# Kernel tuning notes

Hardware: AMD Instinct MI355X
Metric: run time of the kernel (lower is better)

## Reference

```python
import jax, jax.numpy as jnp
import numpy as np

BS, NQ, NC = 128, 900, 91
PRE_TOPK = 10000      # source: pre_topk when n_queries*n_cls > 10000
POST_TOPK = 100       # source: keep_inds[:100]
IOU_THRESH = 0.7


def box_cxcywh_to_xyxy(b):
    cx, cy, w, h = b[..., 0], b[..., 1], b[..., 2], b[..., 3]
    return jnp.stack([cx - 0.5 * w, cy - 0.5 * h, cx + 0.5 * w, cy + 0.5 * h], axis=-1)


def nms_image(boxes, scores, labels):
    """Greedy batched NMS, returning the first POST_TOPK picked indices.
    boxes: [PRE,4] xyxy (scaled), scores: [PRE] desc-sorted, labels: [PRE] int.
    batched_nms trick: offset boxes per class so IoU across classes is 0."""
    max_coord = jnp.max(boxes)
    off = labels.astype(boxes.dtype) * (max_coord + 1.0)
    ob = boxes + off[:, None]                          # [PRE,4]
    areas = (ob[:, 2] - ob[:, 0]) * (ob[:, 3] - ob[:, 1])

    def step(active, _):
        s = jnp.where(active, scores, -jnp.inf)
        i = jnp.argmax(s)                              # highest-score surviving box
        bi = ob[i]
        xx1 = jnp.maximum(bi[0], ob[:, 0])
        yy1 = jnp.maximum(bi[1], ob[:, 1])
        xx2 = jnp.minimum(bi[2], ob[:, 2])
        yy2 = jnp.minimum(bi[3], ob[:, 3])
        inter = jnp.clip(xx2 - xx1, 0.0) * jnp.clip(yy2 - yy1, 0.0)
        union = areas[i] + areas - inter
        iou = inter / jnp.maximum(union, 1e-9)
        # suppress IoU > thresh (includes i itself since iou(i,i)=1)
        active = active & (iou <= IOU_THRESH)
        return active, i

    _, keep = jax.lax.scan(step, jnp.ones(ob.shape[0], dtype=bool), None, length=POST_TOPK)
    return keep                                         # [POST]


def setup_inputs() -> dict:
    key = jax.random.key(0)
    k1, k2, k3, k4 = jax.random.split(key, 4)
    pred_logits = jax.random.normal(k1, (BS, NQ, NC), dtype=jnp.float32) * 2.0 - 2.0
    cxcy = jax.random.uniform(k2, (BS, NQ, 2), dtype=jnp.float32)
    wh = jax.random.uniform(k3, (BS, NQ, 2), dtype=jnp.float32, minval=0.02, maxval=0.3)
    pred_boxes = jnp.concatenate([cxcy, wh], axis=-1)   # cxcywh in [0,1]
    target_sizes = jax.random.uniform(k4, (BS, 2), dtype=jnp.float32, minval=480.0, maxval=1333.0)
    return {"pred_logits": pred_logits, "pred_boxes": pred_boxes, "target_sizes": target_sizes}


def reference(pred_logits, pred_boxes, target_sizes):
    bs, nq, nc = pred_logits.shape
    prob = jax.nn.sigmoid(pred_logits).reshape(bs, nq * nc)      # all_scores
    boxes = box_cxcywh_to_xyxy(pred_boxes)                        # [bs,nq,4]
    img_h, img_w = target_sizes[:, 0], target_sizes[:, 1]
    scale = jnp.stack([img_w, img_h, img_w, img_h], axis=1)       # [bs,4]
    boxes = boxes * scale[:, None, :]

    top_scores, top_idx = jax.lax.top_k(prob, PRE_TOPK)           # [bs,PRE]
    top_labels = top_idx % nc                                     # all_labels gather
    top_box_idx = top_idx // nc                                   # all_boxes gather
    top_boxes = jnp.take_along_axis(boxes, top_box_idx[..., None], axis=1)  # [bs,PRE,4]

    keep = jax.vmap(nms_image)(top_boxes, top_scores, top_labels)  # [bs,POST]
    out_scores = jnp.take_along_axis(top_scores, keep, axis=1)
    out_labels = jnp.take_along_axis(top_labels, keep, axis=1)
    out_boxes = jnp.take_along_axis(top_boxes, keep[..., None], axis=1)
    return out_scores, out_labels, out_boxes
```

## Files before the change

kernel.cpp:

```cpp
#include <hip/hip_runtime.h>
#include <cstdint>

#pragma clang fp contract(off)

#define BS   128
#define NQ   900
#define NC   91
#define NQC  (NQ * NC)
#define Q4   (NQC / 4)
#define HHALF 10238
#define PRE  10000
#define POST 100
#define TBITS 13
#define TBINS (1 << TBITS)
#define TSHIFT (32 - TBITS)
#define K_WIN 16
#define HSEG 1024
#define KS   2780
#define CAPH 7680
#define NSLOT 15

typedef unsigned long long ull;

#define WS_CNT 0
#define WS_GH  4096
#define WS_KEYS (4096 + 4*1024*1024)

__device__ __forceinline__ uint32_t fkey(float f) {
    uint32_t b = __float_as_uint(f);
    return (b & 0x80000000u) ? ~b : (b | 0x80000000u);
}
__device__ __forceinline__ float unkey(uint32_t u) {
    uint32_t b = (u & 0x80000000u) ? (u & 0x7FFFFFFFu) : ~u;
    return __uint_as_float(b);
}
__device__ __forceinline__ uint32_t qclamp(uint32_t q) { return (q < NQ) ? q : (NQ - 1); }

__device__ __forceinline__ ull shflx(ull v, int j) {
    uint32_t lo = (uint32_t)__shfl_xor((int)(uint32_t)v, j, 64);
    uint32_t hi = (uint32_t)__shfl_xor((int)(uint32_t)(v >> 32), j, 64);
    return ((ull)hi << 32) | (ull)lo;
}
__device__ __forceinline__ ull cex(ull v, int j, bool lower, bool desc) {
    ull pb = shflx(v, j);
    ull a = lower ? v : pb;
    ull b = lower ? pb : v;
    bool sw = desc ? (a < b) : (a > b);
    return sw ? pb : v;
}
__device__ __forceinline__ void ce(ull& a, ull& b, bool desc) {
    bool sw = desc ? (a < b) : (a > b);
    if (sw) { ull t = a; a = b; b = t; }
}

__global__ void __launch_bounds__(1024) k_compact(const float* __restrict__ logits,
                                                  ull* __restrict__ keys,
                                                  uint16_t* __restrict__ ghist,
                                                  uint32_t* __restrict__ cnts) {
    const int img = blockIdx.x >> 1;
    const int h = blockIdx.x & 1;
    const int tid = threadIdx.x;
    const int lane = tid & 63;
    __shared__ uint32_t hist[TBINS];
    __shared__ uint32_t part[1024];
    __shared__ uint32_t sTB, sCnt;
    const float4* lg4 = (const float4*)(logits + (size_t)img * NQC);
    for (int i = tid; i < TBINS; i += 1024) hist[i] = 0u;
    if (tid == 0) sCnt = 0u;
    float4 sv[5];
    #pragma unroll
    for (int c = 0; c < 5; ++c) sv[c] = lg4[c * 4096 + tid];
    __syncthreads();
    #pragma unroll
    for (int c = 0; c < 5; ++c) {
        atomicAdd(&hist[fkey(sv[c].x) >> TSHIFT], 1u);
        atomicAdd(&hist[fkey(sv[c].y) >> TSHIFT], 1u);
        atomicAdd(&hist[fkey(sv[c].z) >> TSHIFT], 1u);
        atomicAdd(&hist[fkey(sv[c].w) >> TSHIFT], 1u);
    }
    __syncthreads();
    {
        uint32_t s = 0;
        int b0 = tid * 8;
        #pragma unroll
        for (int j = 0; j < 8; ++j) s += hist[b0 + j];
        part[tid] = s;
    }
    __syncthreads();
    if (tid < 64) {
        uint32_t pv[16]; uint32_t tot = 0;
        #pragma unroll
        for (int j = 0; j < 16; ++j) { pv[j] = part[tid * 16 + j]; tot += pv[j]; }
        uint32_t sinc = tot;
        #pragma unroll
        for (int off = 1; off < 64; off <<= 1) {
            uint32_t o = (uint32_t)__shfl_down((int)sinc, off, 64);
            if (tid + off < 64) sinc += o;
        }
        uint32_t cum = sinc - tot;
        for (int j = 15; j >= 0; --j) {
            if (cum < KS && cum + pv[j] >= KS) {
                int pbn = (tid * 16 + j) * 8;
                uint32_t c2 = cum;
                for (int b = pbn + 7; b >= pbn; --b) {
                    if (c2 + hist[b] >= KS) { sTB = (uint32_t)b; break; }
                    c2 += hist[b];
                }
            }
            cum += pv[j];
        }
    }
    __syncthreads();
    const uint32_t TB = sTB;
    for (int i = tid; i < TBINS; i += 1024) hist[i] = 0u;
    __syncthreads();
    ull* seg = keys + (size_t)(img * 2 + h) * CAPH;
    const int lo = h * HHALF;
    const int hi = (lo + HHALF < Q4) ? (lo + HHALF) : Q4;
    for (int i0 = lo; i0 < hi; i0 += 4096) {
        float4 v[4]; bool inb[4]; int ii[4];
        #pragma unroll
        for (int s = 0; s < 4; ++s) {
            int i = i0 + (s << 10) + tid;
            ii[s] = i; inb[s] = (i < hi);
            v[s] = inb[s] ? lg4[i] : make_float4(0.f, 0.f, 0.f, 0.f);
        }
        uint32_t u[16]; bool pass[16];
        #pragma unroll
        for (int s = 0; s < 4; ++s) {
            u[s * 4 + 0] = fkey(v[s].x); u[s * 4 + 1] = fkey(v[s].y);
            u[s * 4 + 2] = fkey(v[s].z); u[s * 4 + 3] = fkey(v[s].w);
            #pragma unroll
            for (int c = 0; c < 4; ++c)
                pass[s * 4 + c] = inb[s] && ((u[s * 4 + c] >> TSHIFT) >= TB);
        }
        ull m[16]; uint32_t pc[16]; uint32_t tot = 0;
        #pragma unroll
        for (int c = 0; c < 16; ++c) {
            m[c] = __ballot(pass[c]);
            pc[c] = (uint32_t)__popcll(m[c]);
            tot += pc[c];
        }
        uint32_t wb = 0u;
        if (lane == 0 && tot) wb = atomicAdd(&sCnt, tot);
        wb = (uint32_t)__shfl((int)wb, 0, 64);
        ull lm = (1ull << lane) - 1ull;
        uint32_t off = 0;
        #pragma unroll
        for (int c = 0; c < 16; ++c) {
            if (pass[c]) {
                uint32_t p = wb + off + (uint32_t)__popcll(m[c] & lm);
                uint32_t fi = (uint32_t)(ii[c >> 2] * 4 + (c & 3));
                if (p < CAPH) {
                    seg[p] = ((ull)u[c] << 32) | (ull)(0xFFFFFFFFu - fi);
                    atomicAdd(&hist[u[c] >> TSHIFT], 1u);
                }
            }
            off += pc[c];
        }
    }
    __syncthreads();
    uint16_t* g = ghist + (size_t)(img * 2 + h) * TBINS;
    for (int i = tid; i < TBINS; i += 1024) g[i] = (uint16_t)hist[i];
    if (tid == 0) cnts[img * 2 + h] = (sCnt < CAPH) ? sCnt : CAPH;
}

__global__ void __launch_bounds__(1024) k_sel(const ull* __restrict__ keys,
                                              const uint16_t* __restrict__ ghist,
                                              const uint32_t* __restrict__ cnts,
                                              const float* __restrict__ pred_boxes,
                                              const float* __restrict__ target_sizes,
                                              float* __restrict__ out) {
    const int img = blockIdx.x;
    const int tid = threadIdx.x;
    const int lane = tid & 63;
    const int wv = tid >> 6;

    __shared__ uint32_t hist[TBINS];
    __shared__ uint32_t part[1024];
    __shared__ float4 shPB[NQ];
    __shared__ ull binK[HSEG];
    __shared__ ull headK[HSEG];
    __shared__ float aX1[POST], aY1[POST], aX2[POST], aY2[POST], aAr[POST];
    __shared__ int   aCl[POST];
    __shared__ float s_x1[K_WIN], s_y1[K_WIN], s_x2[K_WIN], s_y2[K_WIN];
    __shared__ int   s_cl[K_WIN];
    __shared__ uint32_t s_em[K_WIN];
    __shared__ ull sF0;
    __shared__ uint32_t sCntA, sCntB, sMX;
    __shared__ uint32_t sB1, sTp1, sB2, sTp2, sTK;

    const float ih = target_sizes[img * 2 + 0];
    const float iw = target_sizes[img * 2 + 1];
    const float* pb = pred_boxes + (size_t)img * NQ * 4;

    auto mckey = [&](uint32_t f) -> uint32_t {
        uint32_t q = qclamp(f / NC);
        float4 bb = shPB[q];
        float x1 = (bb.x - 0.5f * bb.z) * iw;
        float y1 = (bb.y - 0.5f * bb.w) * ih;
        float x2 = (bb.x + 0.5f * bb.z) * iw;
        float y2 = (bb.y + 0.5f * bb.w) * ih;
        return fkey(fmaxf(fmaxf(x1, y1), fmaxf(x2, y2)));
    };

    if (tid < NQ) shPB[tid] = ((const float4*)pb)[tid];
    binK[tid] = 0ull; headK[tid] = 0ull;
    if (tid == 0) { sCntA = 0u; sCntB = 0u; sMX = 0u; sF0 = 0ull;
                    sB1 = 0u; sTp1 = 1u; sB2 = 0u; sTp2 = 0u; sTK = 0u; }
    {
        const uint16_t* g0 = ghist + (size_t)(img * 2) * TBINS;
        const uint16_t* g1 = g0 + TBINS;
        uint32_t s = 0;
        int b0 = tid * 8;
        #pragma unroll
        for (int j = 0; j < 8; ++j) {
            uint32_t hv = (uint32_t)g0[b0 + j] + (uint32_t)g1[b0 + j];
            hist[b0 + j] = hv;
            s += hv;
        }
        part[tid] = s;
    }
    const uint32_t c0 = cnts[img * 2 + 0];
    const uint32_t c1 = cnts[img * 2 + 1];
    const int total = (int)(c0 + c1);
    const ull* seg0 = keys + (size_t)(img * 2) * CAPH;
    const ull* seg1 = seg0 + CAPH;
    ull kk[NSLOT];
    #pragma unroll
    for (int j = 0; j < NSLOT; ++j) {
        int i = tid + (j << 10);
        ull x = 0ull;
        if (i < total) x = (i < (int)c0) ? seg0[i] : seg1[i - (int)c0];
        kk[j] = x;
    }
    __syncthreads();

    if (tid < 64) {
        uint32_t pv[16]; uint32_t tot = 0;
        #pragma unroll
        for (int j = 0; j < 16; ++j) { pv[j] = part[tid * 16 + j]; tot += pv[j]; }
        uint32_t sinc = tot;
        #pragma unroll
        for (int off = 1; off < 64; off <<= 1) {
            uint32_t o = (uint32_t)__shfl_down((int)sinc, off, 64);
            if (tid + off < 64) sinc += o;
        }
        uint32_t tt = (uint32_t)__shfl((int)sinc, 0, 64);
        uint32_t TKl = (tt < PRE) ? tt : PRE;
        uint32_t T2l = (TKl < HSEG) ? TKl : HSEG;
        if (tid == 0) sTK = TKl;
        uint32_t cum = sinc - tot;
        for (int j = 15; j >= 0; --j) {
            if (cum < TKl && cum + pv[j] >= TKl) {
                int pbn = (tid * 16 + j) * 8;
                uint32_t c2 = cum;
                for (int b = pbn + 7; b >= pbn; --b) {
                    if (c2 + hist[b] >= TKl) { sB1 = (uint32_t)b; sTp1 = TKl - c2; break; }
                    c2 += hist[b];
                }
            }
            if (cum < T2l && cum + pv[j] >= T2l) {
                int pbn = (tid * 16 + j) * 8;
                uint32_t c2 = cum;
                for (int b = pbn + 7; b >= pbn; --b) {
                    if (c2 + hist[b] >= T2l) { sB2 = (uint32_t)b; sTp2 = T2l - c2; break; }
                    c2 += hist[b];
                }
            }
            cum += pv[j];
        }
    }
    __syncthreads();
    const uint32_t B1 = sB1, tp1 = sTp1, B2 = sB2;
    const uint32_t TK = sTK;
    const int C1 = (int)(((TK < (uint32_t)HSEG) ? TK : (uint32_t)HSEG) - sTp2);

    uint32_t lmx = 0u;
    {
        uint32_t cA = 0u, cB = 0u;
        #pragma unroll
        for (int j = 0; j < NSLOT; ++j) {
            ull x = kk[j];
            uint32_t bin = (uint32_t)(x >> 51);
            bool liveK = (x != 0ull);
            if (liveK && bin > B1) { uint32_t km = mckey(~(uint32_t)x); if (km > lmx) lmx = km; }
            cA += (liveK && bin == B1) ? 1u : 0u;
            cB += (liveK && bin > B2) ? 1u : 0u;
        }
        uint32_t rA = cA, rB = cB;
        #pragma unroll
        for (int off = 32; off > 0; off >>= 1) {
            rA += (uint32_t)__shfl_down((int)rA, off, 64);
            rB += (uint32_t)__shfl_down((int)rB, off, 64);
        }
        if (lane == 0) { part[wv] = rA; part[16 + wv] = rB; }
        __syncthreads();
        if (tid == 0) {
            uint32_t sA = 0u, sB = 0u;
            #pragma unroll
            for (int w = 0; w < 16; ++w) {
                part[32 + w] = sA; sA += part[w];
                part[48 + w] = sB; sB += part[16 + w];
            }
        }
        __syncthreads();
        uint32_t curA = part[32 + wv];
        uint32_t curB = part[48 + wv];
        ull lm = (1ull << lane) - 1ull;
        #pragma unroll
        for (int j = 0; j < NSLOT; ++j) {
            ull x = kk[j];
            uint32_t bin = (uint32_t)(x >> 51);
            bool liveK = (x != 0ull);
            bool isA = liveK && (bin == B1);
            bool isB = liveK && (bin > B2);
            ull mA = __ballot(isA);
            ull mB = __ballot(isB);
            if (isA) {
                uint32_t p = curA + (uint32_t)__popcll(mA & lm);
                if (p < HSEG) binK[p] = x;
            }
            if (isB) {
                uint32_t p = curB + (uint32_t)__popcll(mB & lm);
                if (p < HSEG) headK[p] = x;
            }
            curA += (uint32_t)__popcll(mA);
            curB += (uint32_t)__popcll(mB);
        }
    }
    __syncthreads();

    {
        ull r0 = 0, r1 = 0, r2 = 0, r3 = 0;
        const int cw = wv & 3;
        const int cb = cw << 8;
        ull* A = (wv < 4) ? binK : headK;
        if (wv < 8) {
            r0 = A[cb | lane]; r1 = A[cb | 64 | lane];
            r2 = A[cb | 128 | lane]; r3 = A[cb | 192 | lane];
            #pragma unroll
            for (int k2 = 2; k2 <= 32; k2 <<= 1) {
                bool d = ((lane & k2) == 0);
                #pragma unroll
                for (int j = 16; j >= 1; j >>= 1) {
                    if (j <= (k2 >> 1)) {
                        bool lw = ((lane & j) == 0);
                        r0 = cex(r0, j, lw, d); r1 = cex(r1, j, lw, d);
                        r2 = cex(r2, j, lw, d); r3 = cex(r3, j, lw, d);
                    }
                }
            }
            #pragma unroll
            for (int j = 32; j >= 1; j >>= 1) {
                bool lw = ((lane & j) == 0);
                r0 = cex(r0, j, lw, true);  r1 = cex(r1, j, lw, false);
                r2 = cex(r2, j, lw, true);  r3 = cex(r3, j, lw, false);
            }
            ce(r0, r1, true); ce(r2, r3, false);
            #pragma unroll
            for (int j = 32; j >= 1; j >>= 1) {
                bool lw = ((lane & j) == 0);
                r0 = cex(r0, j, lw, true);  r1 = cex(r1, j, lw, true);
                r2 = cex(r2, j, lw, false); r3 = cex(r3, j, lw, false);
            }
            {
                bool d = ((cw & 1) == 0);
                ce(r0, r2, d); ce(r1, r3, d); ce(r0, r1, d); ce(r2, r3, d);
                #pragma unroll
                for (int j = 32; j >= 1; j >>= 1) {
                    bool lw = ((lane & j) == 0);
                    r0 = cex(r0, j, lw, d); r1 = cex(r1, j, lw, d);
                    r2 = cex(r2, j, lw, d); r3 = cex(r3, j, lw, d);
                }
            }
            A[cb | lane] = r0; A[cb | 64 | lane] = r1;
            A[cb | 128 | lane] = r2; A[cb | 192 | lane] = r3;
        }
        __syncthreads();
        {
            ull* Bp = (tid >> 9) ? headK : binK;
            int t = tid & 511;
            int i = ((t & ~255) << 1) | (t & 255);
            int ixj = i | 256;
            bool d = ((i & 512) == 0);
            ull a = Bp[i], b = Bp[ixj];
            bool sw = d ? (a < b) : (a > b);
            if (sw) { Bp[i] = b; Bp[ixj] = a; }
        }
        __syncthreads();
        if (wv < 8) {
            r0 = A[cb | lane]; r1 = A[cb | 64 | lane];
            r2 = A[cb | 128 | lane]; r3 = A[cb | 192 | lane];
            bool d = ((cw & 2) == 0);
            ce(r0, r2, d); ce(r1, r3, d); ce(r0, r1, d); ce(r2, r3, d);
            #pragma unroll
            for (int j = 32; j >= 1; j >>= 1) {
                bool lw = ((lane & j) == 0);
                r0 = cex(r0, j, lw, d); r1 = cex(r1, j, lw, d);
                r2 = cex(r2, j, lw, d); r3 = cex(r3, j, lw, d);
            }
            A[cb | lane] = r0; A[cb | 64 | lane] = r1;
            A[cb | 128 | lane] = r2; A[cb | 192 | lane] = r3;
        }
        __syncthreads();
        {
            ull* Bp = (tid >> 9) ? headK : binK;
            int t = tid & 511;
            ull a = Bp[t], b = Bp[t | 512];
            if (a < b) { Bp[t] = b; Bp[t | 512] = a; }
        }
        __syncthreads();
        {
            ull* Bp = (tid >> 9) ? headK : binK;
            int t = tid & 511;
            int i = ((t & ~255) << 1) | (t & 255);
            int ixj = i | 256;
            ull a = Bp[i], b = Bp[ixj];
            if (a < b) { Bp[i] = b; Bp[ixj] = a; }
        }
        __syncthreads();
        if (wv < 8) {
            r0 = A[cb | lane]; r1 = A[cb | 64 | lane];
            r2 = A[cb | 128 | lane]; r3 = A[cb | 192 | lane];
            ce(r0, r2, true); ce(r1, r3, true); ce(r0, r1, true); ce(r2, r3, true);
            #pragma unroll
            for (int j = 32; j >= 1; j >>= 1) {
                bool lw = ((lane & j) == 0);
                r0 = cex(r0, j, lw, true); r1 = cex(r1, j, lw, true);
                r2 = cex(r2, j, lw, true); r3 = cex(r3, j, lw, true);
            }
            A[cb | lane] = r0; A[cb | 64 | lane] = r1;
            A[cb | 128 | lane] = r2; A[cb | 192 | lane] = r3;
        }
        __syncthreads();
    }

    if (tid < (int)tp1) {
        ull x = binK[tid];
        if (x != 0ull) { uint32_t km = mckey(~(uint32_t)x); if (km > lmx) lmx = km; }
    }
    for (int off = 32; off > 0; off >>= 1) {
        uint32_t o = (uint32_t)__shfl_down((int)lmx, off, 64);
        if (o > lmx) lmx = o;
    }
    if (lane == 0) atomicMax(&sMX, lmx);
    if (tid == 0 && C1 > 0) sF0 = headK[0];
    __syncthreads();
    float offD;
    {
        uint32_t m = sMX;
        uint32_t b = (m & 0x80000000u) ? (m & 0x7FFFFFFFu) : ~m;
        offD = __uint_as_float(b) + 1.0f;
    }

    auto sort1024 = [&]() {
        const int idx = tid;
        ull x = headK[idx];
        #pragma unroll
        for (int k2 = 2; k2 <= 32; k2 <<= 1) {
            bool d = ((lane & k2) == 0);
            #pragma unroll
            for (int j = 16; j >= 1; j >>= 1)
                if (j <= (k2 >> 1)) x = cex(x, j, (lane & j) == 0, d);
        }
        {
            bool d = ((idx & 64) == 0);
            #pragma unroll
            for (int j = 32; j >= 1; j >>= 1) x = cex(x, j, (lane & j) == 0, d);
        }
        for (int k = 128; k <= 1024; k <<= 1) {
            headK[idx] = x;
            __syncthreads();
            for (int j = k >> 1; j >= 64; j >>= 1) {
                if (tid < 512) {
                    int i2 = ((tid & ~(j - 1)) << 1) | (tid & (j - 1));
                    int ixj = i2 | j;
                    ull a = headK[i2], b = headK[ixj];
                    bool sw = ((i2 & k) == 0) ? (a < b) : (a > b);
                    if (sw) { headK[i2] = b; headK[ixj] = a; }
                }
                __syncthreads();
            }
            x = headK[idx];
            bool d = ((idx & k) == 0);
            #pragma unroll
            for (int j = 32; j >= 1; j >>= 1) x = cex(x, j, (lane & j) == 0, d);
        }
        headK[idx] = x;
        __syncthreads();
    };

    int npick = 0, base = 0, segbase = 0, segend = C1;
    int bcur = (int)B2;
    bool needF0 = (C1 == 0);
    while (npick < POST) {
        if (base >= segend) {
            if (segend >= (int)TK) {
                ull x0 = sF0;
                uint32_t f0 = ~(uint32_t)x0;
                uint32_t u0 = (uint32_t)(x0 >> 32);
                uint32_t q0 = qclamp(f0 / NC);
                uint32_t cc0 = f0 - (f0 / NC) * NC;
                float4 bb = shPB[q0];
                float rx1 = (bb.x - 0.5f * bb.z) * iw;
                float ry1 = (bb.y - 0.5f * bb.w) * ih;
                float rx2 = (bb.x + 0.5f * bb.z) * iw;
                float ry2 = (bb.y + 0.5f * bb.w) * ih;
                float sc = 1.0f / (1.0f + expf(-unkey(u0)));
                for (int p2 = npick + tid; p2 < POST; p2 += 1024) {
                    out[img * POST + p2] = sc;
                    out[BS * POST + img * POST + p2] = (float)cc0;
                    float* ob2 = out + 2 * BS * POST + ((size_t)img * POST + p2) * 4;
                    ob2[0] = rx1; ob2[1] = ry1; ob2[2] = rx2; ob2[3] = ry2;
                }
                break;
            }
            while (bcur > 0 && hist[bcur] == 0u) --bcur;
            headK[tid] = 0ull;
            if (tid == 0) sCntA = 0u;
            __syncthreads();
            for (int i0 = 0; i0 < total; i0 += 1024) {
                int i = i0 + tid;
                ull x = 0ull;
                if (i < total) x = (i < (int)c0) ? seg0[i] : seg1[i - (int)c0];
                bool pass = (x != 0ull) && ((uint32_t)(x >> 51) == (uint32_t)bcur);
                ull m = __ballot(pass);
                if (m) {
                    uint32_t wb = 0u;
                    if (lane == 0) wb = atomicAdd(&sCntA, (uint32_t)__popcll(m));
                    wb = (uint32_t)__shfl((int)wb, 0, 64);
                    if (pass) {
                        uint32_t p = wb + (uint32_t)__popcll(m & ((1ull << lane) - 1ull));
                        if (p < HSEG) headK[p] = x;
                    }
                }
            }
            __syncthreads();
            sort1024();
            int avail = (int)((sCntA < (uint32_t)HSEG) ? sCntA : (uint32_t)HSEG);
            int take = (int)TK - segend; if (take > avail) take = avail;
            if (needF0) { if (tid == 0) sF0 = headK[0]; needF0 = false; __syncthreads(); }
            segbase = segend; segend += take; --bcur;
            continue;
        }

        const int r = base + wv;
        const bool val = (r < segend);
        const ull xk = headK[val ? (r - segbase) : 0];
        const uint32_t f = val ? ~(uint32_t)xk : 0u;
        const uint32_t uk = (uint32_t)(xk >> 32);
        const uint32_t q = qclamp(f / NC);
        const uint32_t cc = f - (f / NC) * NC;
        float4 bb = shPB[q];
        const float x1 = (bb.x - 0.5f * bb.z) * iw;
        const float y1 = (bb.y - 0.5f * bb.w) * ih;
        const float x2 = (bb.x + 0.5f * bb.z) * iw;
        const float y2 = (bb.y + 0.5f * bb.w) * ih;
        if (lane == 0) {
            s_x1[wv] = x1; s_y1[wv] = y1; s_x2[wv] = x2; s_y2[wv] = y2;
            s_cl[wv] = val ? (int)cc : -1;
        }
        __syncthreads();

        const float o = (float)cc * offD;
        const float cx1 = x1 + o, cy1 = y1 + o, cx2 = x2 + o, cy2 = y2 + o;
        const float car = (cx2 - cx1) * (cy2 - cy1);
        bool cf = false;
        if (val && lane < wv && s_cl[lane] == (int)cc) {
            float jx1 = s_x1[lane] + o, jy1 = s_y1[lane] + o;
            float jx2 = s_x2[lane] + o, jy2 = s_y2[lane] + o;
            float arj = (jx2 - jx1) * (jy2 - jy1);
            float xx1 = fmaxf(jx1, cx1), yy1 = fmaxf(jy1, cy1);
            float xx2 = fminf(jx2, cx2), yy2 = fminf(jy2, cy2);
            float inter = fmaxf(xx2 - xx1, 0.0f) * fmaxf(yy2 - yy1, 0.0f);
            float uni = (arj + car) - inter;
            float iou = inter / fmaxf(uni, 1e-9f);
            cf = !(iou <= 0.7f);
        }
        uint32_t em = (uint32_t)(__ballot(cf) & 0xFFFFull);
        bool pf = false;
        for (int i2 = lane; i2 < npick; i2 += 64) {
            if (aCl[i2] == (int)cc) {
                float jx1 = aX1[i2] + o, jy1 = aY1[i2] + o;
                float jx2 = aX2[i2] + o, jy2 = aY2[i2] + o;
                float arj = aAr[i2];
                float xx1 = fmaxf(jx1, cx1), yy1 = fmaxf(jy1, cy1);
                float xx2 = fminf(jx2, cx2), yy2 = fminf(jy2, cy2);
                float inter = fmaxf(xx2 - xx1, 0.0f) * fmaxf(yy2 - yy1, 0.0f);
                float uni = (arj + car) - inter;
                float iou = inter / fmaxf(uni, 1e-9f);
                pf |= !(iou <= 0.7f);
            }
        }
        bool anyPrior = (__ballot(pf) != 0ull);
        if (lane == 0)
            s_em[wv] = em | (anyPrior ? 0x80000000u : 0u) | (val ? 0u : 0x40000000u);
        __syncthreads();

        uint32_t acc = 0u; int a = 0;
        const int room = POST - npick;
        #pragma unroll
        for (int w2 = 0; w2 < K_WIN; ++w2) {
            uint32_t ew = s_em[w2];
            if (!(ew & 0xC0000000u) && a < room && ((ew & 0xFFFFu & acc) == 0u)) {
                acc |= (1u << w2); ++a;
            }
        }

        if (((acc >> wv) & 1u) && lane == 0) {
            int p = npick + __popc(acc & ((1u << wv) - 1u));
            float sc = 1.0f / (1.0f + expf(-unkey(uk)));
            out[img * POST + p] = sc;
            out[BS * POST + img * POST + p] = (float)cc;
            float* ob2 = out + 2 * BS * POST + ((size_t)img * POST + p) * 4;
            ob2[0] = x1; ob2[1] = y1; ob2[2] = x2; ob2[3] = y2;
            aX1[p] = x1; aY1[p] = y1; aX2[p] = x2; aY2[p] = y2;
            aAr[p] = car; aCl[p] = (int)cc;
        }
        npick += a;
        base += K_WIN;
    }
}

extern "C" void kernel_launch(void* const* d_in, const int* in_sizes, int n_in,
                              void* d_out, int out_size, void* d_ws, size_t ws_size,
                              hipStream_t stream) {
    const float* logits = (const float*)d_in[0];
    const float* boxes  = (const float*)d_in[1];
    const float* tsizes = (const float*)d_in[2];
    float* out = (float*)d_out;

    uint32_t* cnts = (uint32_t*)((char*)d_ws + WS_CNT);
    uint16_t* ghist = (uint16_t*)((char*)d_ws + WS_GH);
    ull* keys = (ull*)((char*)d_ws + WS_KEYS);

    k_compact<<<2 * BS, 1024, 0, stream>>>(logits, keys, ghist, cnts);
    k_sel<<<BS, 1024, 0, stream>>>(keys, ghist, cnts, boxes, tsizes, out);
}
```

Measured before the change: 135.1 us.

## Precompute candidate boxes per segment in shared memory and issue key loads early

Decoded box coordinates, class and score key for every head-segment candidate are now computed once per segment into shared arrays. The NMS window loop reads these arrays directly, which removes one per-window barrier and the repeated per-wave decode and division. The global key loads are moved ahead of the histogram setup and split into two fixed 8-slot loops, one per segment, so the loads can overlap the setup. This costs extra shared memory, which may lower occupancy, and adds a trailing barrier at the end of each window iteration.

```diff
diff --git a/kernel.cpp b/kernel.cpp
--- a/kernel.cpp
+++ b/kernel.cpp
@@ -18,7 +18,7 @@
 #define HSEG 1024
 #define KS   2780
 #define CAPH 7680
-#define NSLOT 15
+#define NSLOT 16
 
 typedef unsigned long long ull;
 
@@ -181,10 +181,11 @@
     __shared__ float4 shPB[NQ];
     __shared__ ull binK[HSEG];
     __shared__ ull headK[HSEG];
+    __shared__ float hX1[HSEG], hY1[HSEG], hX2[HSEG], hY2[HSEG];
+    __shared__ int   hCl[HSEG];
+    __shared__ uint32_t hUk[HSEG];
     __shared__ float aX1[POST], aY1[POST], aX2[POST], aY2[POST], aAr[POST];
     __shared__ int   aCl[POST];
-    __shared__ float s_x1[K_WIN], s_y1[K_WIN], s_x2[K_WIN], s_y2[K_WIN];
-    __shared__ int   s_cl[K_WIN];
     __shared__ uint32_t s_em[K_WIN];
     __shared__ ull sF0;
     __shared__ uint32_t sCntA, sCntB, sMX;
@@ -204,6 +205,24 @@
         return fkey(fmaxf(fmaxf(x1, y1), fmaxf(x2, y2)));
     };
 
+    const uint32_t c0 = cnts[img * 2 + 0];
+    const uint32_t c1 = cnts[img * 2 + 1];
+    const ull* seg0 = keys + (size_t)(img * 2) * CAPH;
+    const ull* seg1 = seg0 + CAPH;
+    ull kk[NSLOT];
+    #pragma unroll
+    for (int j = 0; j < 8; ++j) {
+        int i = tid + (j << 10);
+        ull x = (i < CAPH) ? seg0[i] : 0ull;
+        kk[j] = (i < (int)c0) ? x : 0ull;
+    }
+    #pragma unroll
+    for (int j = 0; j < 8; ++j) {
+        int i = tid + (j << 10);
+        ull x = (i < CAPH) ? seg1[i] : 0ull;
+        kk[8 + j] = (i < (int)c1) ? x : 0ull;
+    }
+    const int total = (int)(c0 + c1);
     if (tid < NQ) shPB[tid] = ((const float4*)pb)[tid];
     binK[tid] = 0ull; headK[tid] = 0ull;
     if (tid == 0) { sCntA = 0u; sCntB = 0u; sMX = 0u; sF0 = 0ull;
@@ -220,19 +239,6 @@
             s += hv;
         }
         part[tid] = s;
-    }
-    const uint32_t c0 = cnts[img * 2 + 0];
-    const uint32_t c1 = cnts[img * 2 + 1];
-    const int total = (int)(c0 + c1);
-    const ull* seg0 = keys + (size_t)(img * 2) * CAPH;
-    const ull* seg1 = seg0 + CAPH;
-    ull kk[NSLOT];
-    #pragma unroll
-    for (int j = 0; j < NSLOT; ++j) {
-        int i = tid + (j << 10);
-        ull x = 0ull;
-        if (i < total) x = (i < (int)c0) ? seg0[i] : seg1[i - (int)c0];
-        kk[j] = x;
     }
     __syncthreads();
 
@@ -436,6 +442,21 @@
         __syncthreads();
     }
 
+    auto precomp = [&](int valid_n) {
+        int i = tid;
+        ull xk = headK[i];
+        bool v = (i < valid_n);
+        uint32_t f = v ? ~(uint32_t)xk : 0u;
+        uint32_t q = qclamp(f / NC);
+        float4 bb = shPB[q];
+        hX1[i] = (bb.x - 0.5f * bb.z) * iw;
+        hY1[i] = (bb.y - 0.5f * bb.w) * ih;
+        hX2[i] = (bb.x + 0.5f * bb.z) * iw;
+        hY2[i] = (bb.y + 0.5f * bb.w) * ih;
+        hCl[i] = v ? (int)(f - (f / NC) * NC) : -1;
+        hUk[i] = (uint32_t)(xk >> 32);
+    };
+
     if (tid < (int)tp1) {
         ull x = binK[tid];
         if (x != 0ull) { uint32_t km = mckey(~(uint32_t)x); if (km > lmx) lmx = km; }
@@ -446,6 +467,7 @@
     }
     if (lane == 0) atomicMax(&sMX, lmx);
     if (tid == 0 && C1 > 0) sF0 = headK[0];
+    precomp(C1);
     __syncthreads();
     float offD;
     {
@@ -540,48 +562,43 @@
             sort1024();
             int avail = (int)((sCntA < (uint32_t)HSEG) ? sCntA : (uint32_t)HSEG);
             int take = (int)TK - segend; if (take > avail) take = avail;
-            if (needF0) { if (tid == 0) sF0 = headK[0]; needF0 = false; __syncthreads(); }
+            if (needF0) { if (tid == 0) sF0 = headK[0]; needF0 = false; }
+            precomp(take);
+            __syncthreads();
             segbase = segend; segend += take; --bcur;
             continue;
         }
 
         const int r = base + wv;
         const bool val = (r < segend);
-        const ull xk = headK[val ? (r - segbase) : 0];
-        const uint32_t f = val ? ~(uint32_t)xk : 0u;
-        const uint32_t uk = (uint32_t)(xk >> 32);
-        const uint32_t q = qclamp(f / NC);
-        const uint32_t cc = f - (f / NC) * NC;
-        float4 bb = shPB[q];
-        const float x1 = (bb.x - 0.5f * bb.z) * iw;
-        const float y1 = (bb.y - 0.5f * bb.w) * ih;
-        const float x2 = (bb.x + 0.5f * bb.z) * iw;
-        const float y2 = (bb.y + 0.5f * bb.w) * ih;
-        if (lane == 0) {
-            s_x1[wv] = x1; s_y1[wv] = y1; s_x2[wv] = x2; s_y2[wv] = y2;
-            s_cl[wv] = val ? (int)cc : -1;
-        }
-        __syncthreads();
+        const int li = val ? (r - segbase) : 0;
+        const float x1 = hX1[li], y1 = hY1[li], x2 = hX2[li], y2 = hY2[li];
+        const int ccI = hCl[li];
+        const uint32_t cc = val ? (uint32_t)ccI : 0u;
+        const uint32_t uk = hUk[li];
 
         const float o = (float)cc * offD;
         const float cx1 = x1 + o, cy1 = y1 + o, cx2 = x2 + o, cy2 = y2 + o;
         const float car = (cx2 - cx1) * (cy2 - cy1);
         bool cf = false;
-        if (val && lane < wv && s_cl[lane] == (int)cc) {
-            float jx1 = s_x1[lane] + o, jy1 = s_y1[lane] + o;
-            float jx2 = s_x2[lane] + o, jy2 = s_y2[lane] + o;
-            float arj = (jx2 - jx1) * (jy2 - jy1);
-            float xx1 = fmaxf(jx1, cx1), yy1 = fmaxf(jy1, cy1);
-            float xx2 = fminf(jx2, cx2), yy2 = fminf(jy2, cy2);
-            float inter = fmaxf(xx2 - xx1, 0.0f) * fmaxf(yy2 - yy1, 0.0f);
-            float uni = (arj + car) - inter;
-            float iou = inter / fmaxf(uni, 1e-9f);
-            cf = !(iou <= 0.7f);
+        if (val && lane < wv) {
+            int pl = base + lane - segbase;
+            if (hCl[pl] == (int)cc) {
+                float jx1 = hX1[pl] + o, jy1 = hY1[pl] + o;
+                float jx2 = hX2[pl] + o, jy2 = hY2[pl] + o;
+                float arj = (jx2 - jx1) * (jy2 - jy1);
+                float xx1 = fmaxf(jx1, cx1), yy1 = fmaxf(jy1, cy1);
+                float xx2 = fminf(jx2, cx2), yy2 = fminf(jy2, cy2);
+                float inter = fmaxf(xx2 - xx1, 0.0f) * fmaxf(yy2 - yy1, 0.0f);
+                float uni = (arj + car) - inter;
+                float iou = inter / fmaxf(uni, 1e-9f);
+                cf = !(iou <= 0.7f);
+            }
         }
         uint32_t em = (uint32_t)(__ballot(cf) & 0xFFFFull);
         bool pf = false;
         for (int i2 = lane; i2 < npick; i2 += 64) {
-            if (aCl[i2] == (int)cc) {
+            if (aCl[i2] == (int)cc && val) {
                 float jx1 = aX1[i2] + o, jy1 = aY1[i2] + o;
                 float jx2 = aX2[i2] + o, jy2 = aY2[i2] + o;
                 float arj = aAr[i2];
@@ -620,6 +637,7 @@
         }
         npick += a;
         base += K_WIN;
+        __syncthreads();
     }
 }
 
```

Result: slower. 138.7 us (+2.7%).
